# Optimization experiments

Hardware: AMD Instinct MI355X
Metric: run time of the kernel (lower is better)

The kernel has to match this reference:

```python
import jax, jax.numpy as jnp
import numpy as np

# ---- sign binarization with straight-through estimator (standard BNN) ----
@jax.custom_vjp
def binarize(x):
    return jnp.where(x >= 0, 1.0, -1.0).astype(x.dtype)

def _bin_fwd(x):
    return binarize(x), x

def _bin_bwd(x, g):
    return (g * (jnp.abs(x) <= 1.0).astype(g.dtype),)

binarize.defvjp(_bin_fwd, _bin_bwd)

def conv2d(x, w):
    # x: [N,C,H,W], w: [O,I,kh,kw], stride 1, VALID padding (padding=0)
    return jax.lax.conv_general_dilated(
        x, w, window_strides=(1, 1), padding='VALID',
        dimension_numbers=('NCHW', 'OIHW', 'NCHW'))

def maxpool2(x):
    return jax.lax.reduce_window(x, -jnp.inf, jax.lax.max,
                                 (1, 1, 2, 2), (1, 1, 2, 2), 'VALID')

def hardtanh(x):
    return jnp.clip(x, -1.0, 1.0)

def setup_inputs() -> dict:
    key = jax.random.key(0)
    ks = jax.random.split(key, 11)
    B = 8192
    s = 0.1
    return {
        'x':   jax.random.normal(ks[0], (B, 3, 32, 32), jnp.float32),
        'w1':  jax.random.normal(ks[1], (6, 3, 5, 5), jnp.float32) * s,
        'b1':  jax.random.normal(ks[2], (6,), jnp.float32) * s,
        'w2':  jax.random.normal(ks[3], (16, 6, 5, 5), jnp.float32) * s,
        'b2':  jax.random.normal(ks[4], (16,), jnp.float32) * s,
        'wf1': jax.random.normal(ks[5], (120, 400), jnp.float32) * s,
        'bf1': jax.random.normal(ks[6], (120,), jnp.float32) * s,
        'wf2': jax.random.normal(ks[7], (84, 120), jnp.float32) * s,
        'bf2': jax.random.normal(ks[8], (84,), jnp.float32) * s,
        'wf3': jax.random.normal(ks[9], (10, 84), jnp.float32) * s,
        'bf3': jax.random.normal(ks[10], (10,), jnp.float32) * s,
    }

def reference(x, w1, b1, w2, b2, wf1, bf1, wf2, bf2, wf3, bf3):
    # conv1: first layer -> real-valued input, binarized weights
    out = conv2d(x, binarize(w1)) + b1[None, :, None, None]   # [B,6,28,28]
    out = maxpool2(hardtanh(out))                              # [B,6,14,14]
    # conv2: binarized input and weights
    out = conv2d(binarize(out), binarize(w2)) + b2[None, :, None, None]  # [B,16,10,10]
    out = maxpool2(hardtanh(out))                              # [B,16,5,5]
    out = out.reshape(out.shape[0], -1)                        # [B,400]
    out = hardtanh(binarize(out) @ binarize(wf1).T + bf1)      # [B,120]
    out = hardtanh(binarize(out) @ binarize(wf2).T + bf2)      # [B,84]
    out = binarize(out) @ binarize(wf3).T + bf3                # [B,10]
    return out
```

## Files before the change

kernel.cpp:

```cpp
#include <hip/hip_runtime.h>
#include <stdint.h>

#define TPB 64
#define RCAP 64
#define BAND 0.05f

#define WS_BFR   0
#define WS_W1B   1280
#define WS_W2PK  1298
#define WS_WF1P  1378
#define WS_WF2PK 4378
#define WS_WF3PK 4714

typedef _Float16 half8 __attribute__((ext_vector_type(8)));
typedef float f32x4 __attribute__((ext_vector_type(4)));
typedef unsigned int u32x4 __attribute__((ext_vector_type(4)));

__device__ __forceinline__ uint32_t pkf16(float a, float b) {
  uint32_t lo = (uint32_t)__builtin_bit_cast(uint16_t, (_Float16)a);
  uint32_t hi = (uint32_t)__builtin_bit_cast(uint16_t, (_Float16)b);
  return lo | (hi << 16);
}

__device__ __forceinline__ double win_sum(const float* __restrict__ xb,
                                          uint32_t b0, uint32_t b1, uint32_t b2) {
  double s = 0.0;
#pragma unroll
  for (int ic = 0; ic < 3; ++ic)
#pragma unroll
    for (int rr = 0; rr < 5; ++rr) {
      const float* rp = xb + ic * 1024 + rr * 32;
#pragma unroll
      for (int kc = 0; kc < 5; ++kc) {
        const int idx = ic * 25 + rr * 5 + kc;
        const uint32_t bw = (idx < 32) ? b0 : ((idx < 64) ? b1 : b2);
        double xv = (double)rp[kc];
        s += ((bw >> (idx & 31)) & 1u) ? xv : -xv;
      }
    }
  return s;
}

__global__ __launch_bounds__(256) void prep_kernel(
    const float* __restrict__ w1, const float* __restrict__ w2,
    const float* __restrict__ wf1, const float* __restrict__ wf2,
    const float* __restrict__ wf3, uint32_t* __restrict__ wsu)
{
  int id = blockIdx.x * 256 + threadIdx.x;
  if (id < 1280) {
    int s = id >> 8, r = id & 255, ln = r >> 2, dw = r & 3;
    int g4 = ln >> 4, n = ln & 15;
    int o = 4 * s + g4, r6 = o / 3, cp = o % 3;
    int c = n >> 1, dy = n & 1;
    uint32_t w = 0;
    for (int h = 0; h < 2; ++h) {
      int j2 = dw * 2 + h;
      int ic = j2 & 3, pix = j2 >> 2, kc = cp * 2 + pix, kr = r6 - dy;
      uint32_t f = 0;
      if (n < 12 && o < 18 && ic < 3 && kc < 5 && kr >= 0 && kr <= 4)
        f = (w1[(c * 3 + ic) * 25 + kr * 5 + kc] >= 0.f) ? 0x3C00u : 0xBC00u;
      w |= f << (16 * h);
    }
    wsu[WS_BFR + id] = w;
  } else if (id < 1298) {
    int i = id - 1280, c = i / 3, q = i % 3;
    uint32_t w = 0;
    for (int b = 0; b < 32; ++b) {
      int k = q * 32 + b;
      if (k < 75) w |= (uint32_t)(w1[c*75 + k] >= 0.f) << b;
    }
    wsu[WS_W1B + i] = w;
  } else if (id < 1378) {
    int r = id - 1298, oc = r / 5, kr = r % 5;
    uint32_t w = 0;
    for (int c = 0; c < 6; ++c)
      for (int k = 0; k < 5; ++k)
        w |= (uint32_t)(w2[((oc*6 + c)*5 + kr)*5 + k] >= 0.f) << (5*c + k);
    wsu[WS_W2PK + r] = w;
  } else if (id < 4378) {
    int r = id - 1378, o = r / 25, p = r % 25;
    uint32_t w = 0;
    for (int oc = 0; oc < 16; ++oc)
      w |= (uint32_t)(wf1[o*400 + oc*25 + p] >= 0.f) << oc;
    wsu[WS_WF1P + r] = w;
  } else if (id < 4714) {
    int r = id - 4378, o = r / 4, q = r % 4;
    uint32_t w = 0;
    for (int b = 0; b < 32; ++b) {
      int n = q*32 + b;
      if (n < 120) w |= (uint32_t)(wf2[o*120 + n] >= 0.f) << b;
    }
    wsu[WS_WF2PK + r] = w;
  } else if (id < 4744) {
    int r = id - 4714, o = r / 3, q = r % 3;
    uint32_t w = 0;
    for (int b = 0; b < 32; ++b) {
      int n = q*32 + b;
      if (n < 84) w |= (uint32_t)(wf3[o*84 + n] >= 0.f) << b;
    }
    wsu[WS_WF3PK + r] = w;
  }
}

__global__ void __launch_bounds__(TPB, 4) lenet_kernel(
    const float* __restrict__ x,
    const float* __restrict__ b1, const float* __restrict__ b2,
    const float* __restrict__ bf1, const float* __restrict__ bf2,
    const float* __restrict__ bf3,
    const uint32_t* __restrict__ wsu,
    float* __restrict__ out)
{
  __shared__ __align__(16) union Ovl {
    uint32_t imgh[2112];
    uint32_t ppatch[10][10][5];
  } ovl;
  __shared__ uint32_t w2pks[16][5];
  __shared__ uint32_t w1bs[18];
  __shared__ float sb1[6];
  __shared__ float sb2[16];
  __shared__ uint32_t bits1[6][14];
  __shared__ uint32_t border_[6][14];
  __shared__ uint32_t bits2[25];
  __shared__ uint32_t bitsf1[4];
  __shared__ uint32_t bitsf2[3];
  __shared__ uint32_t rlist[RCAP];
  __shared__ int rcnt;

  const int t = threadIdx.x;
  const int m16 = t & 15;
  const int g4 = t >> 4;
  const long long img = blockIdx.x;

  u32x4 bf[5];
#pragma unroll
  for (int s = 0; s < 5; ++s)
    bf[s] = *(const u32x4*)&wsu[WS_BFR + (s << 8) + (t << 2)];
  int koffs[5];
#pragma unroll
  for (int s = 0; s < 5; ++s) {
    const int o = 4 * s + g4;
    koffs[s] = (o < 18) ? (o / 3) * 33 + (o % 3) * 2 : 0;
  }

  {
    const int y = t >> 1, xh = t & 1;
    const float* rp = x + img * 3072 + y * 32 + xh * 16;
    const int pixbase = y * 33 + xh * 16;
#pragma unroll
    for (int q = 0; q < 4; ++q) {
      float4 f0 = *(const float4*)(rp +    0 + 4 * q);
      float4 f1 = *(const float4*)(rp + 1024 + 4 * q);
      float4 f2 = *(const float4*)(rp + 2048 + 4 * q);
      uint32_t* d = &ovl.imgh[2 * (pixbase + 4 * q)];
      *(uint2*)(d + 0) = make_uint2(pkf16(f0.x, f1.x), pkf16(f2.x, 0.f));
      *(uint2*)(d + 2) = make_uint2(pkf16(f0.y, f1.y), pkf16(f2.y, 0.f));
      *(uint2*)(d + 4) = make_uint2(pkf16(f0.z, f1.z), pkf16(f2.z, 0.f));
      *(uint2*)(d + 6) = make_uint2(pkf16(f0.w, f1.w), pkf16(f2.w, 0.f));
    }
    if (t < 32)
      *(uint2*)&ovl.imgh[2 * (t * 33 + 32)] = make_uint2(0u, 0u);
    for (int id = t; id < 80; id += TPB) w2pks[id / 5][id % 5] = wsu[WS_W2PK + id];
    if (t < 18) w1bs[t] = wsu[WS_W1B + t];
    if (t < 6)  sb1[t] = b1[t];
    if (t >= 32 && t < 48) sb2[t - 32] = b2[t - 32];
    for (int id = t; id < 84; id += TPB) {
      ((uint32_t*)bits1)[id] = 0; ((uint32_t*)border_)[id] = 0;
    }
    if (t < 25) bits2[t] = 0;
    if (t >= 25 && t < 29) bitsf1[t - 25] = 0;
    if (t >= 29 && t < 32) bitsf2[t - 29] = 0;
    if (t == 63) rcnt = 0;
  }
  __syncthreads();

  {
    const int n = m16;
    const int c = n >> 1;
    const float bcr = sb1[(n < 12) ? c : 0];
    for (int pyi = 0; pyi < 14; ++pyi) {
      const int rowpix = (2 * pyi) * 33 + m16;
      f32x4 aX = {0.f, 0.f, 0.f, 0.f}, aY = {0.f, 0.f, 0.f, 0.f};
#pragma unroll
      for (int s = 0; s < 5; ++s) {
        const uint2* pX = (const uint2*)&ovl.imgh[2 * (rowpix + koffs[s])];
        const uint2* pY = (const uint2*)&ovl.imgh[2 * (rowpix + 12 + koffs[s])];
        uint2 x0 = pX[0], x1 = pX[1];
        uint2 y0 = pY[0], y1 = pY[1];
        u32x4 wa = {x0.x, x0.y, x1.x, x1.y};
        u32x4 wb = {y0.x, y0.y, y1.x, y1.y};
        aX = __builtin_amdgcn_mfma_f32_16x16x32_f16(
               __builtin_bit_cast(half8, wa), __builtin_bit_cast(half8, bf[s]), aX, 0, 0, 0);
        aY = __builtin_amdgcn_mfma_f32_16x16x32_f16(
               __builtin_bit_cast(half8, wb), __builtin_bit_cast(half8, bf[s]), aY, 0, 0, 0);
      }
      float pX0 = fmaxf(aX[0], aX[1]), pX1 = fmaxf(aX[2], aX[3]);
      float pY0 = fmaxf(aY[0], aY[1]), pY1 = fmaxf(aY[2], aY[3]);
      float qX0 = fmaxf(pX0, __shfl_xor(pX0, 1));
      float qX1 = fmaxf(pX1, __shfl_xor(pX1, 1));
      float qY0 = fmaxf(pY0, __shfl_xor(pY0, 1));
      float qY1 = fmaxf(pY1, __shfl_xor(pY1, 1));
      uint32_t comb = 0;
      {
        float v0 = qX0 + bcr, v1 = qX1 + bcr, v2 = qY0 + bcr, v3 = qY1 + bcr;
        const int p0 = g4 * 2, p1 = g4 * 2 + 1, p2 = 6 + g4 * 2, p3 = 7 + g4 * 2;
        if (fabsf(v0) < BAND) comb |= 1u << (16 + p0); else if (v0 >= 0.f) comb |= 1u << p0;
        if (fabsf(v1) < BAND) comb |= 1u << (16 + p1); else if (v1 >= 0.f) comb |= 1u << p1;
        if (fabsf(v2) < BAND) comb |= 1u << (16 + p2); else if (v2 >= 0.f) comb |= 1u << p2;
        if (fabsf(v3) < BAND) comb |= 1u << (16 + p3); else if (v3 >= 0.f) comb |= 1u << p3;
      }
      comb |= __shfl_xor(comb, 16);
      comb |= __shfl_xor(comb, 32);
      if (g4 == 0 && n < 12 && (n & 1) == 0) {
        bits1[c][pyi]   = comb & 0x3FFFu;
        border_[c][pyi] = comb >> 16;
      }
    }
  }
  __syncthreads();

  for (int id = t; id < 84; id += TPB) {
    uint32_t bw = ((uint32_t*)border_)[id];
    while (bw) {
      int pj = __ffs(bw) - 1;
      bw &= bw - 1;
      int slot = atomicAdd(&rcnt, 1);
      if (slot < RCAP) rlist[slot] = (uint32_t)(id * 16 + pj);
    }
  }
  __syncthreads();

  {
    const int cnt = min(rcnt, RCAP);
    for (int k = t; k < cnt * 4; k += TPB) {
      const int e = k >> 2, win = k & 3;
      const uint32_t ent = rlist[e];
      const int pj = ent & 15, w = ent >> 4;
      const int pi = w % 14, c = w / 14;
      const int dr = win >> 1, dc = win & 1;
      const float* xb = x + img * 3072 + (2*pi + dr) * 32 + (2*pj + dc);
      double s = win_sum(xb, w1bs[c*3], w1bs[c*3+1], w1bs[c*3+2]);
      double s1 = fmax(s, __shfl_xor(s, 1));
      double sm = fmax(s1, __shfl_xor(s1, 2));
      if (win == 0) {
        if (sm + (double)sb1[c] >= 0.0)
          atomicOr(&((uint32_t*)bits1)[w], 1u << pj);
      }
    }
    if (rcnt > RCAP) {
      for (int id = t; id < 1176; id += TPB) {
        const int w = id / 14, pj = id % 14;
        if ((((uint32_t*)border_)[w] >> pj) & 1u) {
          const int pi = w % 14, c = w / 14;
          double best = -1e300;
          for (int dr = 0; dr < 2; ++dr)
            for (int dc = 0; dc < 2; ++dc) {
              const float* xb = x + img * 3072 + (2*pi + dr) * 32 + (2*pj + dc);
              double s = win_sum(xb, w1bs[c*3], w1bs[c*3+1], w1bs[c*3+2]);
              best = best > s ? best : s;
            }
          if (best + (double)sb1[c] >= 0.0)
            atomicOr(&((uint32_t*)bits1)[w], 1u << pj);
        }
      }
    }
  }
  __syncthreads();

  for (int id = t; id < 500; id += TPB) {
    const int kr = id % 5;
    const int ij = id / 5;
    const int i = ij / 10, j = ij % 10;
    uint32_t w = 0;
#pragma unroll
    for (int c = 0; c < 6; ++c)
      w |= ((bits1[c][i + kr] >> j) & 31u) << (5*c);
    ovl.ppatch[i][j][kr] = w;
  }
  __syncthreads();

  for (int id = t; id < 400; id += TPB) {
    const int oc  = id / 25;
    const int pos = id % 25;
    const int pi = pos / 5, pj = pos % 5;
    int dmin = 1000;
#pragma unroll
    for (int dy = 0; dy < 2; ++dy)
#pragma unroll
      for (int dx = 0; dx < 2; ++dx) {
        const uint32_t* pp = ovl.ppatch[2*pi + dy][2*pj + dx];
        int d = 0;
#pragma unroll
        for (int kr = 0; kr < 5; ++kr) d += __popc(pp[kr] ^ w2pks[oc][kr]);
        dmin = min(dmin, d);
      }
    float v = (float)(150 - 2*dmin) + sb2[oc];
    if (v >= 0.f) atomicOr(&bits2[pos], 1u << oc);
  }
  __syncthreads();

  for (int id = t; id < 120; id += TPB) {
    const int o = id;
    const uint32_t* wrow = wsu + WS_WF1P + o*25;
    int d = 0;
#pragma unroll
    for (int p = 0; p < 25; ++p) d += __popc(bits2[p] ^ wrow[p]);
    float v = (float)(400 - 2*d) + bf1[o];
    if (v >= 0.f) atomicOr(&bitsf1[o >> 5], 1u << (o & 31));
  }
  __syncthreads();

  for (int id = t; id < 84; id += TPB) {
    const int o = id;
    int d = 0;
#pragma unroll
    for (int q = 0; q < 4; ++q)
      d += __popc(bitsf1[q] ^ wsu[WS_WF2PK + o*4 + q]);
    float v = (float)(120 - 2*d) + bf2[o];
    if (v >= 0.f) atomicOr(&bitsf2[o >> 5], 1u << (o & 31));
  }
  __syncthreads();

  if (t < 10) {
    const int o = t;
    int d = 0;
#pragma unroll
    for (int q = 0; q < 3; ++q)
      d += __popc(bitsf2[q] ^ wsu[WS_WF3PK + o*3 + q]);
    out[img*10 + o] = (float)(84 - 2*d) + bf3[o];
  }
}

extern "C" void kernel_launch(void* const* d_in, const int* in_sizes, int n_in,
                              void* d_out, int out_size, void* d_ws, size_t ws_size,
                              hipStream_t stream)
{
  const float* x   = (const float*)d_in[0];
  const float* w1  = (const float*)d_in[1];
  const float* b1  = (const float*)d_in[2];
  const float* w2  = (const float*)d_in[3];
  const float* b2  = (const float*)d_in[4];
  const float* wf1 = (const float*)d_in[5];
  const float* bf1 = (const float*)d_in[6];
  const float* wf2 = (const float*)d_in[7];
  const float* bf2 = (const float*)d_in[8];
  const float* wf3 = (const float*)d_in[9];
  const float* bf3 = (const float*)d_in[10];
  uint32_t* wsu = (uint32_t*)d_ws;

  const int imgs = in_sizes[0] / 3072;
  hipLaunchKernelGGL(prep_kernel, dim3(19), dim3(256), 0, stream,
                     w1, w2, wf1, wf2, wf3, wsu);
  hipLaunchKernelGGL(lenet_kernel, dim3(imgs), dim3(TPB), 0, stream,
                     x, b1, b2, bf1, bf2, bf3, wsu, (float*)d_out);
}
```

Before: 67.16 us.

## Restructure conv2 and FC tail into register/ballot stages with fewer barriers

Conv2 patch building moves into registers: each lane owns two adjacent output columns and finds the 2x2 pool max through a partner-lane shuffle, removing the ppatch pass and one barrier. The FC layers produce their binarized outputs with wave ballots instead of shared-memory atomics, so the last three barriers are dropped. Weight and bias staging in LDS is replaced by direct global/scalar loads, the quad shuffle in conv1 becomes a DPP move, and workspace offsets are shifted for alignment. LDS use shrinks, but there are more redundant global reads of small weight tables per thread.

```diff
diff --git a/kernel.cpp b/kernel.cpp
--- a/kernel.cpp
+++ b/kernel.cpp
@@ -9,8 +9,8 @@
 #define WS_W1B   1280
 #define WS_W2PK  1298
 #define WS_WF1P  1378
-#define WS_WF2PK 4378
-#define WS_WF3PK 4714
+#define WS_WF2PK 4380
+#define WS_WF3PK 4716
 
 typedef _Float16 half8 __attribute__((ext_vector_type(8)));
 typedef float f32x4 __attribute__((ext_vector_type(4)));
@@ -20,6 +20,11 @@
   uint32_t lo = (uint32_t)__builtin_bit_cast(uint16_t, (_Float16)a);
   uint32_t hi = (uint32_t)__builtin_bit_cast(uint16_t, (_Float16)b);
   return lo | (hi << 16);
+}
+
+__device__ __forceinline__ float qpswap(float v) {
+  return __builtin_bit_cast(float, __builtin_amdgcn_mov_dpp(
+      __builtin_bit_cast(int, v), 0xB1, 0xF, 0xF, true));
 }
 
 __device__ __forceinline__ double win_sum(const float* __restrict__ xb,
@@ -83,16 +88,16 @@
     for (int oc = 0; oc < 16; ++oc)
       w |= (uint32_t)(wf1[o*400 + oc*25 + p] >= 0.f) << oc;
     wsu[WS_WF1P + r] = w;
-  } else if (id < 4714) {
-    int r = id - 4378, o = r / 4, q = r % 4;
+  } else if (id >= 4380 && id < 4716) {
+    int r = id - 4380, o = r / 4, q = r % 4;
     uint32_t w = 0;
     for (int b = 0; b < 32; ++b) {
       int n = q*32 + b;
       if (n < 120) w |= (uint32_t)(wf2[o*120 + n] >= 0.f) << b;
     }
     wsu[WS_WF2PK + r] = w;
-  } else if (id < 4744) {
-    int r = id - 4714, o = r / 3, q = r % 3;
+  } else if (id >= 4716 && id < 4746) {
+    int r = id - 4716, o = r / 3, q = r % 3;
     uint32_t w = 0;
     for (int b = 0; b < 32; ++b) {
       int n = q*32 + b;
@@ -110,19 +115,10 @@
     const uint32_t* __restrict__ wsu,
     float* __restrict__ out)
 {
-  __shared__ __align__(16) union Ovl {
-    uint32_t imgh[2112];
-    uint32_t ppatch[10][10][5];
-  } ovl;
-  __shared__ uint32_t w2pks[16][5];
-  __shared__ uint32_t w1bs[18];
-  __shared__ float sb1[6];
-  __shared__ float sb2[16];
+  __shared__ __align__(16) uint32_t imgh[2112];
   __shared__ uint32_t bits1[6][14];
   __shared__ uint32_t border_[6][14];
-  __shared__ uint32_t bits2[25];
-  __shared__ uint32_t bitsf1[4];
-  __shared__ uint32_t bitsf2[3];
+  __shared__ uint32_t bits2s[25];
   __shared__ uint32_t rlist[RCAP];
   __shared__ int rcnt;
 
@@ -131,10 +127,10 @@
   const int g4 = t >> 4;
   const long long img = blockIdx.x;
 
-  u32x4 bf[5];
+  u32x4 bfr[5];
 #pragma unroll
   for (int s = 0; s < 5; ++s)
-    bf[s] = *(const u32x4*)&wsu[WS_BFR + (s << 8) + (t << 2)];
+    bfr[s] = *(const u32x4*)&wsu[WS_BFR + (s << 8) + (t << 2)];
   int koffs[5];
 #pragma unroll
   for (int s = 0; s < 5; ++s) {
@@ -151,54 +147,44 @@
       float4 f0 = *(const float4*)(rp +    0 + 4 * q);
       float4 f1 = *(const float4*)(rp + 1024 + 4 * q);
       float4 f2 = *(const float4*)(rp + 2048 + 4 * q);
-      uint32_t* d = &ovl.imgh[2 * (pixbase + 4 * q)];
+      uint32_t* d = &imgh[2 * (pixbase + 4 * q)];
       *(uint2*)(d + 0) = make_uint2(pkf16(f0.x, f1.x), pkf16(f2.x, 0.f));
       *(uint2*)(d + 2) = make_uint2(pkf16(f0.y, f1.y), pkf16(f2.y, 0.f));
       *(uint2*)(d + 4) = make_uint2(pkf16(f0.z, f1.z), pkf16(f2.z, 0.f));
       *(uint2*)(d + 6) = make_uint2(pkf16(f0.w, f1.w), pkf16(f2.w, 0.f));
     }
     if (t < 32)
-      *(uint2*)&ovl.imgh[2 * (t * 33 + 32)] = make_uint2(0u, 0u);
-    for (int id = t; id < 80; id += TPB) w2pks[id / 5][id % 5] = wsu[WS_W2PK + id];
-    if (t < 18) w1bs[t] = wsu[WS_W1B + t];
-    if (t < 6)  sb1[t] = b1[t];
-    if (t >= 32 && t < 48) sb2[t - 32] = b2[t - 32];
-    for (int id = t; id < 84; id += TPB) {
-      ((uint32_t*)bits1)[id] = 0; ((uint32_t*)border_)[id] = 0;
-    }
-    if (t < 25) bits2[t] = 0;
-    if (t >= 25 && t < 29) bitsf1[t - 25] = 0;
-    if (t >= 29 && t < 32) bitsf2[t - 29] = 0;
-    if (t == 63) rcnt = 0;
+      *(uint2*)&imgh[2 * (t * 33 + 32)] = make_uint2(0u, 0u);
+    if (t == 0) rcnt = 0;
   }
   __syncthreads();
 
   {
     const int n = m16;
     const int c = n >> 1;
-    const float bcr = sb1[(n < 12) ? c : 0];
+    const float bcr = b1[(n < 12) ? c : 0];
     for (int pyi = 0; pyi < 14; ++pyi) {
       const int rowpix = (2 * pyi) * 33 + m16;
       f32x4 aX = {0.f, 0.f, 0.f, 0.f}, aY = {0.f, 0.f, 0.f, 0.f};
 #pragma unroll
       for (int s = 0; s < 5; ++s) {
-        const uint2* pX = (const uint2*)&ovl.imgh[2 * (rowpix + koffs[s])];
-        const uint2* pY = (const uint2*)&ovl.imgh[2 * (rowpix + 12 + koffs[s])];
+        const uint2* pX = (const uint2*)&imgh[2 * (rowpix + koffs[s])];
+        const uint2* pY = (const uint2*)&imgh[2 * (rowpix + 12 + koffs[s])];
         uint2 x0 = pX[0], x1 = pX[1];
         uint2 y0 = pY[0], y1 = pY[1];
         u32x4 wa = {x0.x, x0.y, x1.x, x1.y};
         u32x4 wb = {y0.x, y0.y, y1.x, y1.y};
         aX = __builtin_amdgcn_mfma_f32_16x16x32_f16(
-               __builtin_bit_cast(half8, wa), __builtin_bit_cast(half8, bf[s]), aX, 0, 0, 0);
+               __builtin_bit_cast(half8, wa), __builtin_bit_cast(half8, bfr[s]), aX, 0, 0, 0);
         aY = __builtin_amdgcn_mfma_f32_16x16x32_f16(
-               __builtin_bit_cast(half8, wb), __builtin_bit_cast(half8, bf[s]), aY, 0, 0, 0);
+               __builtin_bit_cast(half8, wb), __builtin_bit_cast(half8, bfr[s]), aY, 0, 0, 0);
       }
       float pX0 = fmaxf(aX[0], aX[1]), pX1 = fmaxf(aX[2], aX[3]);
       float pY0 = fmaxf(aY[0], aY[1]), pY1 = fmaxf(aY[2], aY[3]);
-      float qX0 = fmaxf(pX0, __shfl_xor(pX0, 1));
-      float qX1 = fmaxf(pX1, __shfl_xor(pX1, 1));
-      float qY0 = fmaxf(pY0, __shfl_xor(pY0, 1));
-      float qY1 = fmaxf(pY1, __shfl_xor(pY1, 1));
+      float qX0 = fmaxf(pX0, qpswap(pX0));
+      float qX1 = fmaxf(pX1, qpswap(pX1));
+      float qY0 = fmaxf(pY0, qpswap(pY0));
+      float qY1 = fmaxf(pY1, qpswap(pY1));
       uint32_t comb = 0;
       {
         float v0 = qX0 + bcr, v1 = qX1 + bcr, v2 = qY0 + bcr, v3 = qY1 + bcr;
@@ -238,11 +224,11 @@
       const int pi = w % 14, c = w / 14;
       const int dr = win >> 1, dc = win & 1;
       const float* xb = x + img * 3072 + (2*pi + dr) * 32 + (2*pj + dc);
-      double s = win_sum(xb, w1bs[c*3], w1bs[c*3+1], w1bs[c*3+2]);
+      double s = win_sum(xb, wsu[WS_W1B + c*3], wsu[WS_W1B + c*3+1], wsu[WS_W1B + c*3+2]);
       double s1 = fmax(s, __shfl_xor(s, 1));
       double sm = fmax(s1, __shfl_xor(s1, 2));
       if (win == 0) {
-        if (sm + (double)sb1[c] >= 0.0)
+        if (sm + (double)b1[c] >= 0.0)
           atomicOr(&((uint32_t*)bits1)[w], 1u << pj);
       }
     }
@@ -255,10 +241,10 @@
           for (int dr = 0; dr < 2; ++dr)
             for (int dc = 0; dc < 2; ++dc) {
               const float* xb = x + img * 3072 + (2*pi + dr) * 32 + (2*pj + dc);
-              double s = win_sum(xb, w1bs[c*3], w1bs[c*3+1], w1bs[c*3+2]);
+              double s = win_sum(xb, wsu[WS_W1B + c*3], wsu[WS_W1B + c*3+1], wsu[WS_W1B + c*3+2]);
               best = best > s ? best : s;
             }
-          if (best + (double)sb1[c] >= 0.0)
+          if (best + (double)b1[c] >= 0.0)
             atomicOr(&((uint32_t*)bits1)[w], 1u << pj);
         }
       }
@@ -266,67 +252,93 @@
   }
   __syncthreads();
 
-  for (int id = t; id < 500; id += TPB) {
-    const int kr = id % 5;
-    const int ij = id / 5;
-    const int i = ij / 10, j = ij % 10;
-    uint32_t w = 0;
-#pragma unroll
-    for (int c = 0; c < 6; ++c)
-      w |= ((bits1[c][i + kr] >> j) & 31u) << (5*c);
-    ovl.ppatch[i][j][kr] = w;
-  }
-  __syncthreads();
-
-  for (int id = t; id < 400; id += TPB) {
-    const int oc  = id / 25;
-    const int pos = id % 25;
-    const int pi = pos / 5, pj = pos % 5;
-    int dmin = 1000;
-#pragma unroll
-    for (int dy = 0; dy < 2; ++dy)
-#pragma unroll
-      for (int dx = 0; dx < 2; ++dx) {
-        const uint32_t* pp = ovl.ppatch[2*pi + dy][2*pj + dx];
-        int d = 0;
-#pragma unroll
-        for (int kr = 0; kr < 5; ++kr) d += __popc(pp[kr] ^ w2pks[oc][kr]);
-        dmin = min(dmin, d);
-      }
-    float v = (float)(150 - 2*dmin) + sb2[oc];
-    if (v >= 0.f) atomicOr(&bits2[pos], 1u << oc);
-  }
-  __syncthreads();
-
-  for (int id = t; id < 120; id += TPB) {
-    const int o = id;
-    const uint32_t* wrow = wsu + WS_WF1P + o*25;
-    int d = 0;
-#pragma unroll
-    for (int p = 0; p < 25; ++p) d += __popc(bits2[p] ^ wrow[p]);
-    float v = (float)(400 - 2*d) + bf1[o];
-    if (v >= 0.f) atomicOr(&bitsf1[o >> 5], 1u << (o & 31));
-  }
-  __syncthreads();
-
-  for (int id = t; id < 84; id += TPB) {
-    const int o = id;
-    int d = 0;
-#pragma unroll
-    for (int q = 0; q < 4; ++q)
-      d += __popc(bitsf1[q] ^ wsu[WS_WF2PK + o*4 + q]);
-    float v = (float)(120 - 2*d) + bf2[o];
-    if (v >= 0.f) atomicOr(&bitsf2[o >> 5], 1u << (o & 31));
-  }
-  __syncthreads();
+  {
+    const int la  = (t < 50) ? t : 49;
+    const int i   = la / 5;
+    const int pjc = la % 5;
+    const int j0  = 2 * pjc;
+    uint32_t ppA[5], ppB[5];
+#pragma unroll
+    for (int kr = 0; kr < 5; ++kr) {
+      uint32_t wa = 0, wb = 0;
+#pragma unroll
+      for (int c = 0; c < 6; ++c) {
+        uint32_t bc = bits1[c][i + kr];
+        wa |= ((bc >> j0) & 31u) << (5*c);
+        wb |= ((bc >> (j0 + 1)) & 31u) << (5*c);
+      }
+      ppA[kr] = wa; ppB[kr] = wb;
+    }
+    const int partner = (i & 1) ? (la - 5) : (la + 5);
+    uint32_t myword = 0;
+#pragma unroll 4
+    for (int oc = 0; oc < 16; ++oc) {
+      int dA = 0, dB = 0;
+#pragma unroll
+      for (int kr = 0; kr < 5; ++kr) {
+        const uint32_t wv = wsu[WS_W2PK + oc*5 + kr];
+        dA += __popc(ppA[kr] ^ wv);
+        dB += __popc(ppB[kr] ^ wv);
+      }
+      int dm = min(dA, dB);
+      int dp = __shfl(dm, partner);
+      int dmin = min(dm, dp);
+      float v = (float)(150 - 2*dmin) + b2[oc];
+      myword |= (v >= 0.f ? 1u : 0u) << oc;
+    }
+    if (t < 50 && (i & 1) == 0) bits2s[(i >> 1) * 5 + pjc] = myword;
+  }
+  __syncthreads();
+
+  uint32_t f1w0, f1w1, f1w2, f1w3;
+  {
+    uint32_t p2[25];
+#pragma unroll
+    for (int p = 0; p < 25; ++p) p2[p] = bits2s[p];
+    const uint32_t* wrA = wsu + WS_WF1P + t * 25;
+    int d1 = 0;
+#pragma unroll
+    for (int p = 0; p < 25; ++p) d1 += __popc(p2[p] ^ wrA[p]);
+    float v1 = (float)(400 - 2*d1) + bf1[t];
+    const bool act2 = (t < 56);
+    const int o2 = 64 + t;
+    int d2 = 0;
+    const uint32_t* wrB = wsu + WS_WF1P + o2 * 25;
+    if (act2) {
+#pragma unroll
+      for (int p = 0; p < 25; ++p) d2 += __popc(p2[p] ^ wrB[p]);
+    }
+    float v2 = act2 ? ((float)(400 - 2*d2) + bf1[o2]) : -1.f;
+    unsigned long long mA = __ballot(v1 >= 0.f);
+    unsigned long long mB = __ballot(act2 && (v2 >= 0.f));
+    f1w0 = (uint32_t)mA; f1w1 = (uint32_t)(mA >> 32);
+    f1w2 = (uint32_t)mB; f1w3 = (uint32_t)(mB >> 32);
+  }
+
+  uint32_t f2w0, f2w1, f2w2;
+  {
+    const uint32_t* wr = wsu + WS_WF2PK + t * 4;
+    int d3 = __popc(f1w0 ^ wr[0]) + __popc(f1w1 ^ wr[1]) +
+             __popc(f1w2 ^ wr[2]) + __popc(f1w3 ^ wr[3]);
+    float v3 = (float)(120 - 2*d3) + bf2[t];
+    const bool act4 = (t < 20);
+    const int o4 = 64 + t;
+    const uint32_t* wr2 = wsu + WS_WF2PK + o4 * 4;
+    int d4 = 0;
+    if (act4)
+      d4 = __popc(f1w0 ^ wr2[0]) + __popc(f1w1 ^ wr2[1]) +
+           __popc(f1w2 ^ wr2[2]) + __popc(f1w3 ^ wr2[3]);
+    float v4 = act4 ? ((float)(120 - 2*d4) + bf2[o4]) : -1.f;
+    unsigned long long mC = __ballot(v3 >= 0.f);
+    unsigned long long mD = __ballot(act4 && (v4 >= 0.f));
+    f2w0 = (uint32_t)mC; f2w1 = (uint32_t)(mC >> 32); f2w2 = (uint32_t)mD;
+  }
 
   if (t < 10) {
-    const int o = t;
-    int d = 0;
-#pragma unroll
-    for (int q = 0; q < 3; ++q)
-      d += __popc(bitsf2[q] ^ wsu[WS_WF3PK + o*3 + q]);
-    out[img*10 + o] = (float)(84 - 2*d) + bf3[o];
+    int d = __popc(f2w0 ^ wsu[WS_WF3PK + t*3 + 0]) +
+            __popc(f2w1 ^ wsu[WS_WF3PK + t*3 + 1]) +
+            __popc(f2w2 ^ wsu[WS_WF3PK + t*3 + 2]);
+    out[img*10 + t] = (float)(84 - 2*d) + bf3[t];
   }
 }
 
```

Result: faster. 61.92 us (-7.8%).
